# Kernel tuning notes

Measured on AMD Instinct MI355X. Metric: run time of the kernel, lower is better.

## Reference

```python
import jax, jax.numpy as jnp
import numpy as np

H = 16        # num_attention_heads
E = 1024      # hidden_size
D = E // H    # attention_head_size = 64
M = 1024      # max_position_embeddings
EPS = 1e-12


def setup_inputs() -> dict:
    key = jax.random.key(0)
    ks = jax.random.split(key, 12)
    s = 0.02
    B, S = 8, 1024
    return {
        "hidden_states": jax.random.normal(ks[0], (B, S, E), jnp.float32),
        "Wq": jax.random.normal(ks[1], (E, E), jnp.float32) * s,
        "bq": jnp.zeros((E,), jnp.float32),
        "Wk": jax.random.normal(ks[2], (E, E), jnp.float32) * s,
        "bk": jnp.zeros((E,), jnp.float32),
        "Wv": jax.random.normal(ks[3], (E, E), jnp.float32) * s,
        "bv": jnp.zeros((E,), jnp.float32),
        "dist_emb": jax.random.normal(ks[4], (2 * M - 1, D), jnp.float32) * s,
        "Wo": jax.random.normal(ks[5], (E, E), jnp.float32) * s,
        "bo": jnp.zeros((E,), jnp.float32),
        "ln_gamma": jnp.ones((E,), jnp.float32),
        "ln_beta": jnp.zeros((E,), jnp.float32),
    }


def reference(hidden_states, Wq, bq, Wk, bk, Wv, bv, dist_emb, Wo, bo, ln_gamma, ln_beta):
    B, S, _ = hidden_states.shape

    def heads(x):  # [B,S,E] -> [B,H,S,D]
        return x.reshape(B, S, H, D).transpose(0, 2, 1, 3)

    q = heads(hidden_states @ Wq + bq)
    k = heads(hidden_states @ Wk + bk)
    v = heads(hidden_states @ Wv + bv)

    scores = jnp.einsum("bhqd,bhkd->bhqk", q, k)

    # relative_key_query positional bias
    pos_l = jnp.arange(S)[:, None]
    pos_r = jnp.arange(S)[None, :]
    dist_idx = pos_l - pos_r + M - 1            # [S,S] in [0, 2M-2]
    pos_emb = dist_emb[dist_idx]                # [S,S,D]  (l, r, d)
    rel_q = jnp.einsum("bhld,lrd->bhlr", q, pos_emb)
    rel_k = jnp.einsum("bhrd,lrd->bhlr", k, pos_emb)
    scores = (scores + rel_q + rel_k) / jnp.sqrt(jnp.asarray(D, scores.dtype))

    probs = jax.nn.softmax(scores, axis=-1)     # dropout prob = 0 (eval)
    ctx = jnp.einsum("bhqk,bhkd->bhqd", probs, v)
    ctx = ctx.transpose(0, 2, 1, 3).reshape(B, S, E)

    # BertSelfOutput: dense + residual + LayerNorm
    h = ctx @ Wo + bo + hidden_states
    mu = jnp.mean(h, axis=-1, keepdims=True)
    var = jnp.mean(jnp.square(h - mu), axis=-1, keepdims=True)
    out = (h - mu) * jax.lax.rsqrt(var + EPS) * ln_gamma + ln_beta
    return out
```

## Files before the change

kernel.cpp:

```cpp
#include <hip/hip_runtime.h>


typedef unsigned short u16;
typedef unsigned int u32;
typedef unsigned long long u64;
typedef __bf16 bf16x8 __attribute__((ext_vector_type(8)));
typedef float  f32x4  __attribute__((ext_vector_type(4)));
typedef int    i32x4  __attribute__((ext_vector_type(4)));

__device__ __forceinline__ float b2f(u16 u) {
  union { u32 i; float f; } x;
  x.i = ((u32)u) << 16;
  return x.f;
}
__device__ __forceinline__ u16 f2b_manual(float f) {
  union { float f; u32 u; } x;
  x.f = f;
  return (u16)((x.u + 0x7FFFu + ((x.u >> 16) & 1u)) >> 16);
}
#if __has_builtin(__builtin_amdgcn_cvt_pk_bf16_f32)
typedef __bf16 bf16x2 __attribute__((ext_vector_type(2)));
__device__ __forceinline__ u32 cvt2(float a, float b) {
  union { bf16x2 v; u32 u; } x;
  x.v = __builtin_amdgcn_cvt_pk_bf16_f32(a, b);
  return x.u;
}
#else
__device__ __forceinline__ u32 cvt2(float a, float b) {
  return (u32)f2b_manual(a) | ((u32)f2b_manual(b) << 16);
}
#endif
__device__ __forceinline__ u16 f2b(float f) { return (u16)(cvt2(f, f) & 0xffffu); }

union LdU { i32x4 i4; bf16x8 b8; };
__device__ __forceinline__ bf16x8 ldb8(const u16* p) {
  LdU u; u.i4 = *(const i32x4*)p; return u.b8;
}
__device__ __forceinline__ void pack8(u16* dst, const float* src) {
  f32x4 lo = *(const f32x4*)src, hi = *(const f32x4*)(src + 4);
  i32x4 v;
  v.x = (int)cvt2(lo.x, lo.y); v.y = (int)cvt2(lo.z, lo.w);
  v.z = (int)cvt2(hi.x, hi.y); v.w = (int)cvt2(hi.z, hi.w);
  *(i32x4*)dst = v;
}
#define MFMA16(a, b, c) __builtin_amdgcn_mfma_f32_16x16x32_bf16((a), (b), (c), 0, 0, 0)

template <int C>
__device__ __forceinline__ float dppmov(float x) {
  union { float f; int i; } a, r;
  a.f = x;
  r.i = __builtin_amdgcn_update_dpp(0, a.i, C, 0xF, 0xF, true);
  return r.f;
}
__device__ __forceinline__ float rsum16(float x) {
  x += dppmov<0xB1>(x);
  x += dppmov<0x4E>(x);
  x += dppmov<0x141>(x);
  x += dppmov<0x140>(x);
  return x;
}
__device__ __forceinline__ float fexp2(float x) {
#if __has_builtin(__builtin_amdgcn_exp2f)
  return __builtin_amdgcn_exp2f(x);
#else
  return exp2f(x);
#endif
}

#if __has_builtin(__builtin_amdgcn_global_load_lds)
#define HAS_GLDS 1
typedef __attribute__((address_space(3))) u32 as3_u32;
typedef const __attribute__((address_space(1))) u32 as1_u32;
__device__ __forceinline__ void gld16(const u16* g, u16* lds_wave_base) {
  __builtin_amdgcn_global_load_lds(
      (as1_u32*)g, (as3_u32*)(u32)(u64)lds_wave_base, 16, 0, 0);
}
#else
#define HAS_GLDS 0
__device__ __forceinline__ void gld16_fb(const u16* g, u16* lds_wave_base,
                                         int lane) {
  *(i32x4*)(lds_wave_base + lane * 8) = *(const i32x4*)g;
}
#endif

#define SQRT_C2 0.42466090f

__global__ __launch_bounds__(256) void convX(
    const float* __restrict__ X, u16* __restrict__ Xb) {
  int i = (blockIdx.x * 256 + threadIdx.x) * 8;
  pack8(&Xb[i], &X[i]);
}

__global__ __launch_bounds__(256) void convD(
    const float* __restrict__ dist, u16* __restrict__ distb) {
  int i = (blockIdx.x * 256 + threadIdx.x) * 8;
  if (i < 2047 * 64) {
    float t[8];
#pragma unroll
    for (int j = 0; j < 8; j++) t[j] = dist[i + j] * SQRT_C2;
    pack8(&distb[i], t);
  }
}

__global__ __launch_bounds__(256) void convWt4(
    const float* __restrict__ W0, const float* __restrict__ W1,
    const float* __restrict__ W2, const float* __restrict__ W3,
    u16* __restrict__ Wt) {
  __shared__ float tile[64][65];
  const int tid = threadIdx.x;
  const int k0 = blockIdx.x * 64, m0 = blockIdx.y * 64;
  const int z = blockIdx.z;
  const float* W = (z == 0) ? W0 : (z == 1) ? W1 : (z == 2) ? W2 : W3;
  u16* Wtz = Wt + (size_t)z * 1024 * 1024;
#pragma unroll
  for (int it = 0; it < 4; it++) {
    int row = (tid >> 4) + 16 * it;
    int col = (tid & 15) * 4;
    f32x4 v = *(const f32x4*)&W[(size_t)(k0 + row) * 1024 + m0 + col];
    tile[row][col] = v.x; tile[row][col + 1] = v.y;
    tile[row][col + 2] = v.z; tile[row][col + 3] = v.w;
  }
  __syncthreads();
#pragma unroll
  for (int it = 0; it < 4; it++) {
    int mr = (tid >> 4) + 16 * it;
    int kc = (tid & 15) * 4;
    u32 w0 = cvt2(tile[kc][mr], tile[kc + 1][mr]);
    u32 w1 = cvt2(tile[kc + 2][mr], tile[kc + 3][mr]);
    *(u64*)&Wtz[(size_t)(m0 + mr) * 1024 + k0 + kc] = (u64)w0 | ((u64)w1 << 32);
  }
}

__global__ __launch_bounds__(256) void transV(
    const u16* __restrict__ V, u16* __restrict__ Vt) {
  __shared__ u16 tile[64][72];
  const int tid = threadIdx.x;
  const int bh = blockIdx.y, b = bh >> 4, h = bh & 15;
  const int s0 = blockIdx.x << 6;
  const u16* Vb = V + (size_t)(b * 1024) * 1024 + h * 64;
  {
    int rp = tid >> 3, a = tid & 7;
    const u16* src = &Vb[(size_t)(s0 + 2 * rp) * 1024 + a * 8];
    i32x4 va = *(const i32x4*)src;
    i32x4 vb2 = *(const i32x4*)(src + 1024);
    u16 ta[8] __attribute__((aligned(16)));
    u16 tb[8] __attribute__((aligned(16)));
    *(i32x4*)ta = va; *(i32x4*)tb = vb2;
    int colb = ((((rp >> 2) ^ a) << 3) | ((2 * rp) & 7));
#pragma unroll
    for (int j = 0; j < 8; j++)
      *(u32*)&tile[a * 8 + j][colb] = (u32)ta[j] | ((u32)tb[j] << 16);
  }
  __syncthreads();
  int d = tid >> 2, cc = tid & 3;
  int sw = (d >> 3) & 7;
  i32x4 lo = *(const i32x4*)&tile[d][((2 * cc) ^ sw) << 3];
  i32x4 hi = *(const i32x4*)&tile[d][((2 * cc + 1) ^ sw) << 3];
  u16* dst = Vt + ((size_t)bh * 64 + d) * 1024 + s0 + cc * 16;
  *(i32x4*)dst = lo;
  *(i32x4*)(dst + 8) = hi;
}

template <int RESID, int OUTF32, int QKV>
__global__ __launch_bounds__(256) void gemm_bb(
    const u16* __restrict__ A, const u16* __restrict__ Wt,
    const float* __restrict__ bias, const float* __restrict__ biasK,
    const float* __restrict__ biasV, const float* __restrict__ resid,
    float* __restrict__ outF, u16* __restrict__ outB, int N, int K, int M) {
  __shared__ u16 sA[128 * 64];
  __shared__ u16 sW[128 * 64];

  const int tid = threadIdx.x;
  const int lane = tid & 63, w = tid >> 6;
  const int quad = lane >> 4, lb = lane & 15;
  const int m0 = blockIdx.y * 128, n0 = blockIdx.x * 128;

  const int srow = lane >> 3;
  const int gcol = ((lane & 7) ^ srow) << 3;

  f32x4 acc[2][8] = {};

  for (int k0 = 0; k0 < K; k0 += 64) {
#pragma unroll
    for (int j = 0; j < 4; j++) {
      int rb = (4 * w + j) * 8;
      const u16* ga = &A[(size_t)(n0 + rb + srow) * K + k0 + gcol];
      const u16* gw = &Wt[(size_t)(m0 + rb + srow) * K + k0 + gcol];
#if HAS_GLDS
      gld16(ga, &sA[rb * 64]);
      gld16(gw, &sW[rb * 64]);
#else
      gld16_fb(ga, &sA[rb * 64], lane);
      gld16_fb(gw, &sW[rb * 64], lane);
#endif
    }
    __syncthreads();

    const int r0 = 32 * w + lb;
    const int sw0 = r0 & 7;
    bf16x8 a00 = ldb8(&sA[r0 * 64 + ((quad ^ sw0) << 3)]);
    bf16x8 a01 = ldb8(&sA[r0 * 64 + (((4 + quad) ^ sw0) << 3)]);
    bf16x8 a10 = ldb8(&sA[(r0 + 16) * 64 + ((quad ^ sw0) << 3)]);
    bf16x8 a11 = ldb8(&sA[(r0 + 16) * 64 + (((4 + quad) ^ sw0) << 3)]);
#pragma unroll
    for (int t = 0; t < 8; t++) {
      int n = 16 * t + lb;
      int swn = n & 7;
      bf16x8 b0 = ldb8(&sW[n * 64 + ((quad ^ swn) << 3)]);
      bf16x8 b1 = ldb8(&sW[n * 64 + (((4 + quad) ^ swn) << 3)]);
      acc[0][t] = MFMA16(a00, b0, acc[0][t]);
      acc[0][t] = MFMA16(a01, b1, acc[0][t]);
      acc[1][t] = MFMA16(a10, b0, acc[1][t]);
      acc[1][t] = MFMA16(a11, b1, acc[1][t]);
    }
    __syncthreads();
  }

  const float* bp = bias;
  u16* outSeg = outB;
  float osc = 1.0f;
  int mbase = m0;
  if (QKV) {
    int seg = m0 >> 10;
    bp = (seg == 0) ? bias : (seg == 1) ? biasK : biasV;
    outSeg = outB + (size_t)seg * ((size_t)8192 * 1024);
    osc = (seg < 2) ? SQRT_C2 : 1.0f;
    mbase = m0 & 1023;
  }

#pragma unroll
  for (int half = 0; half < 2; half++)
#pragma unroll
    for (int t = 0; t < 8; t++) {
      int colw = mbase + 16 * t + lb;
      float bv = bp[colw];
#pragma unroll
      for (int i = 0; i < 4; i++) {
        int rowg = n0 + 32 * w + 16 * half + quad * 4 + i;
        float v = acc[half][t][i] + bv;
        if (RESID) v += resid[(size_t)rowg * M + colw];
        if (QKV) v *= osc;
        if (OUTF32) outF[(size_t)rowg * M + colw] = v;
        else        outSeg[(size_t)rowg * (QKV ? 1024 : M) + colw] = f2b(v);
      }
    }
}

__global__ __launch_bounds__(256) void attn(
    const u16* __restrict__ Q, const u16* __restrict__ Kv,
    const u16* __restrict__ Vt, const u16* __restrict__ distb,
    u16* __restrict__ ctx) {
  __shared__ u16 sQ[64][72];
  __shared__ u16 sK[64][72];
  __shared__ u16 sVt[64][72];
  __shared__ u16 sP[128][72];
  __shared__ u16 sGq[128 * 64];
  __shared__ u16 sGk[128 * 64];

  const int tid = threadIdx.x;
  const int lane = tid & 63, w = tid >> 6;
  const int quad = lane >> 4, lb = lane & 15;
  const int f = blockIdx.y * 16 + blockIdx.x;
  const int xcd = f & 7, slot = f >> 3;
  const int bh = (xcd << 4) | (slot & 15);
  const int q0 = (slot >> 4) << 6;
  const int b = bh >> 4, h = bh & 15;
  const int S = 1024, E = 1024;
  const u16* Qb = Q  + (size_t)(b * S) * E + h * 64;
  const u16* Kb = Kv + (size_t)(b * S) * E + h * 64;
  const u16* Vtb = Vt + (size_t)bh * 64 * 1024;

  const int sr = tid >> 3, sc8 = (tid & 7) << 3;

  {
    *(i32x4*)&sQ[sr][sc8] = *(const i32x4*)&Qb[(size_t)(q0 + sr) * E + sc8];
    *(i32x4*)&sQ[sr + 32][sc8] =
        *(const i32x4*)&Qb[(size_t)(q0 + sr + 32) * E + sc8];
    *(i32x4*)&sK[sr][sc8] = *(const i32x4*)&Kb[(size_t)sr * E + sc8];
    *(i32x4*)&sK[sr + 32][sc8] =
        *(const i32x4*)&Kb[(size_t)(sr + 32) * E + sc8];
    *(i32x4*)&sVt[sr][sc8] = *(const i32x4*)&Vtb[(size_t)sr * 1024 + sc8];
    *(i32x4*)&sVt[sr + 32][sc8] =
        *(const i32x4*)&Vtb[(size_t)(sr + 32) * 1024 + sc8];
    const int dbase = q0 + 960;
#pragma unroll
    for (int j = 0; j < 4; j++) {
      int p = sr + 32 * j;
      int g = dbase + p;
      if (g > 2046) g = 2046;
      *(i32x4*)&sP[p][sc8] = *(const i32x4*)&distb[(size_t)g * 64 + sc8];
    }
  }
  __syncthreads();

  const int row = 16 * w + lb;
  bf16x8 aq0 = ldb8(&sQ[row][quad * 8]);
  bf16x8 aq1 = ldb8(&sQ[row][32 + quad * 8]);

  const u16* kb  = &sK[lb][quad * 8];
  const u16* vbp = &sVt[lb][quad * 8];
  const u16* akb = &sK[row][quad * 8];
  const u16* pb  = &sP[lb][quad * 8];
  u16* gqsb = &sGq[lb * 64 + ((16 * w + 4 * quad) ^ ((lb & 7) << 3))];
  u16* gksb = &sGk[lb * 64 + ((16 * w + 4 * quad) ^ ((lb & 7) << 3))];
  u16* psb  = &sK[16 * w + 4 * quad][lb];
  const int rl_ = 16 * w + 4 * quad;
  const u16* gqa_[4];
  const u16* gka_[4][4];
#pragma unroll
  for (int i = 0; i < 4; i++) {
    int rl = rl_ + i;
    int c3 = rl - lb + 15;
    int sw8 = (c3 & 7) << 3;
    gqa_[i] = &sGq[(c3 << 6) + (rl ^ sw8)];
#pragma unroll
    for (int t = 0; t < 4; t++) {
      int c = rl - (16 * t + lb) + 63;
      gka_[i][t] = &sGk[(c << 6) + ((16 * t + lb) ^ sw8)];
    }
  }
  const u16* kg0 = Kb + (size_t)(64 + sr) * E + sc8;
  const u16* kg1 = kg0 + (size_t)32 * E;
  const u16* vg0 = Vtb + (size_t)sr * 1024 + 64 + sc8;
  const u16* vg1 = vg0 + (size_t)32 * 1024;
  const u16* dg0 = distb + (size_t)(q0 - 64 + 960 + sr) * 64 + sc8;
  const u16* dg1 = dg0 + (size_t)32 * 64;
  u16* wk0 = &sK[sr][sc8];  u16* wk1 = &sK[sr + 32][sc8];
  u16* wv0 = &sVt[sr][sc8]; u16* wv1 = &sVt[sr + 32][sc8];
  u16* wp0 = &sP[sr][sc8];  u16* wp1 = &sP[sr + 32][sc8];

  const int uqlo = w, uqhi = w + 4;
  const int uklo = 3 - w, ukhi = 7 - w;

  f32x4 accO[4] = {};
  float l_i[4] = {0.f, 0.f, 0.f, 0.f};

  for (int kt = 0; kt < 16; kt++) {
    const int xorv = (kt & 1) << 6;

    i32x4 kr0, kr1, vr0, vr1, dr0, dr1;
    if (kt < 15) {
      kr0 = *(const i32x4*)kg0;
      kr1 = *(const i32x4*)kg1;
      vr0 = *(const i32x4*)vg0;
      vr1 = *(const i32x4*)vg1;
      dr0 = *(const i32x4*)dg0;
      dr1 = *(const i32x4*)dg1;
    }

    __builtin_amdgcn_s_setprio(1);
    f32x4 accS[4] = {};
#pragma unroll
    for (int t = 0; t < 4; t++) {
      bf16x8 b0 = ldb8(kb + 1152 * t);
      bf16x8 b1 = ldb8(kb + 1152 * t + 32);
      accS[t] = MFMA16(aq0, b0, accS[t]);
      accS[t] = MFMA16(aq1, b1, accS[t]);
    }
    bf16x8 ak0 = ldb8(akb);
    bf16x8 ak1 = ldb8(akb + 32);
    const u16* pbA = pb + (xorv ? 4608 : 0);
    const u16* pbB = pb + (xorv ? -4608 : 0);
#pragma unroll
    for (int u = 0; u < 8; u++) {
      const bool doq = (u >= uqlo) && (u <= uqhi);
      const bool dok = (u >= uklo) && (u <= ukhi);
      if (doq || dok) {
        const u16* pp = (u < 4 ? pbA : pbB) + 1152 * u;
        bf16x8 p0 = ldb8(pp);
        bf16x8 p1 = ldb8(pp + 32);
        if (doq) {
          f32x4 gq = {};
          gq = MFMA16(aq0, p0, gq);
          gq = MFMA16(aq1, p1, gq);
          *(u32*)(gqsb + 1024 * u) = cvt2(gq[0], gq[1]);
          *(u32*)(gqsb + 1024 * u + 2) = cvt2(gq[2], gq[3]);
        }
        if (dok) {
          f32x4 gk = {};
          gk = MFMA16(ak0, p0, gk);
          gk = MFMA16(ak1, p1, gk);
          *(u32*)(gksb + 1024 * u) = cvt2(gk[0], gk[1]);
          *(u32*)(gksb + 1024 * u + 2) = cvt2(gk[2], gk[3]);
        }
      }
    }
    __builtin_amdgcn_s_setprio(0);
    __syncthreads();

    float pr[4][4];
#pragma unroll
    for (int t = 0; t < 4; t++) {
#pragma unroll
      for (int i = 0; i < 4; i++) {
        float s = accS[t][i] + b2f(gqa_[i][1024 * (3 - t)]) +
                  b2f(*gka_[i][t]);
        float e = fexp2(s);
        pr[t][i] = e;
        l_i[i] += e;
      }
    }

#pragma unroll
    for (int t = 0; t < 4; t++)
#pragma unroll
      for (int i = 0; i < 4; i++)
        psb[72 * i + 16 * t] = f2b(pr[t][i]);

    bf16x8 ap0 = ldb8(akb);
    bf16x8 ap1 = ldb8(akb + 32);
    __builtin_amdgcn_s_setprio(1);
#pragma unroll
    for (int t = 0; t < 4; t++) {
      bf16x8 v0 = ldb8(vbp + 1152 * t);
      bf16x8 v1 = ldb8(vbp + 1152 * t + 32);
      accO[t] = MFMA16(ap0, v0, accO[t]);
      accO[t] = MFMA16(ap1, v1, accO[t]);
    }
    __builtin_amdgcn_s_setprio(0);
    __syncthreads();

    if (kt < 15) {
      const int pxn = ((kt + 1) & 1) ? 4608 : 0;
      *(i32x4*)wk0 = kr0;
      *(i32x4*)wk1 = kr1;
      *(i32x4*)wv0 = vr0;
      *(i32x4*)wv1 = vr1;
      *(i32x4*)(wp0 + pxn) = dr0;
      *(i32x4*)(wp1 + pxn) = dr1;
      kg0 += (size_t)64 * E; kg1 += (size_t)64 * E;
      vg0 += 64;             vg1 += 64;
      dg0 -= 64 * 64;        dg1 -= 64 * 64;
      __syncthreads();
    }
  }

#pragma unroll
  for (int i = 0; i < 4; i++) l_i[i] = rsum16(l_i[i]);

  u16* Cb = ctx + (size_t)(b * S) * E + h * 64;
#pragma unroll
  for (int t = 0; t < 4; t++)
#pragma unroll
    for (int i = 0; i < 4; i++) {
      int rl = 16 * w + quad * 4 + i;
      Cb[(size_t)(q0 + rl) * E + 16 * t + lb] = f2b(accO[t][i] / l_i[i]);
    }
}

__global__ __launch_bounds__(256) void lnorm(
    const float* __restrict__ Hp, const float* __restrict__ gamma,
    const float* __restrict__ beta, float* __restrict__ out) {
  __shared__ float red[8];
  const int rowb = blockIdx.x, tid = threadIdx.x;
  const float* hr = Hp + (size_t)rowb * 1024;
  f32x4 v = *(const f32x4*)&hr[tid * 4];
  float s = v.x + v.y + v.z + v.w;
  float q = v.x * v.x + v.y * v.y + v.z * v.z + v.w * v.w;
#pragma unroll
  for (int d = 1; d < 64; d <<= 1) {
    s += __shfl_xor(s, d, 64);
    q += __shfl_xor(q, d, 64);
  }
  int w = tid >> 6, lane = tid & 63;
  if (lane == 0) { red[w] = s; red[4 + w] = q; }
  __syncthreads();
  s = red[0] + red[1] + red[2] + red[3];
  q = red[4] + red[5] + red[6] + red[7];
  float mu = s * (1.f / 1024.f);
  float var = q * (1.f / 1024.f) - mu * mu;
  float rstd = rsqrtf(var + 1e-12f);
  float* orow = out + (size_t)rowb * 1024;
  f32x4 o;
#pragma unroll
  for (int j = 0; j < 4; j++) {
    int c = tid * 4 + j;
    o[j] = (v[j] - mu) * rstd * gamma[c] + beta[c];
  }
  *(f32x4*)&orow[tid * 4] = o;
}

extern "C" void kernel_launch(void* const* d_in, const int* in_sizes, int n_in,
                              void* d_out, int out_size, void* d_ws,
                              size_t ws_size, hipStream_t stream) {
  const float* X    = (const float*)d_in[0];
  const float* Wq   = (const float*)d_in[1];
  const float* bq   = (const float*)d_in[2];
  const float* Wk   = (const float*)d_in[3];
  const float* bk   = (const float*)d_in[4];
  const float* Wv   = (const float*)d_in[5];
  const float* bv   = (const float*)d_in[6];
  const float* dist = (const float*)d_in[7];
  const float* Wo   = (const float*)d_in[8];
  const float* bo   = (const float*)d_in[9];
  const float* gam  = (const float*)d_in[10];
  const float* bet  = (const float*)d_in[11];

  const size_t NE = (size_t)8192 * 1024;
  char* ws = (char*)d_ws;
  u16* Qw = (u16*)(ws);
  u16* Kw = (u16*)(ws + 2 * NE);
  u16* Vw = (u16*)(ws + 4 * NE);
  u16* Cw = (u16*)(ws + 6 * NE);
  float* Hp = (float*)ws;

  char* ob = (char*)d_out;
  u16* Wt4 = (u16*)(ob);
  u16* Wto = (u16*)(ob + (6u << 20));
  u16* Xb  = (u16*)(ob + (8u << 20));
  u16* Vtg = (u16*)(ob + (8u << 20));
  u16* distb = (u16*)(ob + (26u << 20));

  dim3 bb(256);
  convWt4<<<dim3(16, 16, 4), bb, 0, stream>>>(Wq, Wk, Wv, Wo, Wt4);
  convX<<<dim3(4096), bb, 0, stream>>>(X, Xb);
  convD<<<dim3(64), bb, 0, stream>>>(dist, distb);

  gemm_bb<0, 0, 1><<<dim3(64, 24), bb, 0, stream>>>(
      Xb, Wt4, bq, bk, bv, nullptr, nullptr, Qw, 8192, 1024, 3072);
  transV<<<dim3(16, 128), bb, 0, stream>>>(Vw, Vtg);
  attn<<<dim3(16, 128), bb, 0, stream>>>(Qw, Kw, Vtg, distb, Cw);
  gemm_bb<1, 1, 0><<<dim3(64, 8), bb, 0, stream>>>(
      Cw, Wto, bo, nullptr, nullptr, X, Hp, nullptr, 8192, 1024, 1024);
  lnorm<<<dim3(8192), bb, 0, stream>>>(Hp, gam, bet, (float*)d_out);
}
```

Baseline: 406.5 us.

## Shrink attention LDS footprint via XOR-swizzled layouts and aliased Q buffer

Replaces the padded [64][72] layouts of V^T and the distance-embedding tile with unpadded 64-wide rows that use an XOR swizzle to avoid bank conflicts. The Gq/Gk scratch shrinks from 128 to 80 rows by offsetting per-wave indices, and the Q staging buffer is aliased onto sGk because Q is only read once into registers. The smaller shared-memory footprint is meant to let more blocks reside per CU. The risk is indexing errors in the rebased Gq/Gk offsets and the aliasing.

```diff
diff --git a/kernel.cpp b/kernel.cpp
--- a/kernel.cpp
+++ b/kernel.cpp
@@ -250,12 +250,11 @@
     const u16* __restrict__ Q, const u16* __restrict__ Kv,
     const u16* __restrict__ Vt, const u16* __restrict__ distb,
     u16* __restrict__ ctx) {
-  __shared__ u16 sQ[64][72];
   __shared__ u16 sK[64][72];
-  __shared__ u16 sVt[64][72];
-  __shared__ u16 sP[128][72];
-  __shared__ u16 sGq[128 * 64];
-  __shared__ u16 sGk[128 * 64];
+  __shared__ u16 sVt[64 * 64];
+  __shared__ u16 sP[128 * 64];
+  __shared__ u16 sGq[80 * 64];
+  __shared__ u16 sGk[80 * 64];
 
   const int tid = threadIdx.x;
   const int lane = tid & 63, w = tid >> 6;
@@ -270,17 +269,19 @@
   const u16* Kb = Kv + (size_t)(b * S) * E + h * 64;
   const u16* Vtb = Vt + (size_t)bh * 64 * 1024;
 
-  const int sr = tid >> 3, sc8 = (tid & 7) << 3;
+  const int sr = tid >> 3, g8 = tid & 7, sc8 = g8 << 3;
+  const int vswz = (g8 ^ (sr & 7)) << 3;
 
   {
+    u16(*sQ)[72] = (u16(*)[72])sGk;
     *(i32x4*)&sQ[sr][sc8] = *(const i32x4*)&Qb[(size_t)(q0 + sr) * E + sc8];
     *(i32x4*)&sQ[sr + 32][sc8] =
         *(const i32x4*)&Qb[(size_t)(q0 + sr + 32) * E + sc8];
     *(i32x4*)&sK[sr][sc8] = *(const i32x4*)&Kb[(size_t)sr * E + sc8];
     *(i32x4*)&sK[sr + 32][sc8] =
         *(const i32x4*)&Kb[(size_t)(sr + 32) * E + sc8];
-    *(i32x4*)&sVt[sr][sc8] = *(const i32x4*)&Vtb[(size_t)sr * 1024 + sc8];
-    *(i32x4*)&sVt[sr + 32][sc8] =
+    *(i32x4*)&sVt[sr * 64 + vswz] = *(const i32x4*)&Vtb[(size_t)sr * 1024 + sc8];
+    *(i32x4*)&sVt[(sr + 32) * 64 + vswz] =
         *(const i32x4*)&Vtb[(size_t)(sr + 32) * 1024 + sc8];
     const int dbase = q0 + 960;
 #pragma unroll
@@ -288,21 +289,29 @@
       int p = sr + 32 * j;
       int g = dbase + p;
       if (g > 2046) g = 2046;
-      *(i32x4*)&sP[p][sc8] = *(const i32x4*)&distb[(size_t)g * 64 + sc8];
+      *(i32x4*)&sP[p * 64 + vswz] = *(const i32x4*)&distb[(size_t)g * 64 + sc8];
     }
   }
   __syncthreads();
 
   const int row = 16 * w + lb;
-  bf16x8 aq0 = ldb8(&sQ[row][quad * 8]);
-  bf16x8 aq1 = ldb8(&sQ[row][32 + quad * 8]);
-
-  const u16* kb  = &sK[lb][quad * 8];
-  const u16* vbp = &sVt[lb][quad * 8];
+  bf16x8 aq0, aq1;
+  {
+    u16(*sQ)[72] = (u16(*)[72])sGk;
+    aq0 = ldb8(&sQ[row][quad * 8]);
+    aq1 = ldb8(&sQ[row][32 + quad * 8]);
+  }
+
+  const int lsw = (lb & 7) << 3;
+  const u16* kb   = &sK[lb][quad * 8];
+  const u16* vbp0 = &sVt[lb * 64 + ((quad ^ (lb & 7)) << 3)];
+  const u16* vbp1 = &sVt[lb * 64 + (((4 + quad) ^ (lb & 7)) << 3)];
   const u16* akb = &sK[row][quad * 8];
-  const u16* pb  = &sP[lb][quad * 8];
-  u16* gqsb = &sGq[lb * 64 + ((16 * w + 4 * quad) ^ ((lb & 7) << 3))];
-  u16* gksb = &sGk[lb * 64 + ((16 * w + 4 * quad) ^ ((lb & 7) << 3))];
+  const u16* pb0 = &sP[lb * 64 + ((quad ^ (lb & 7)) << 3)];
+  const u16* pb1 = &sP[lb * 64 + (((4 + quad) ^ (lb & 7)) << 3)];
+  const int cswz = (16 * w + 4 * quad) ^ lsw;
+  u16* gqsb = sGq + (lb * 64 + cswz - 1024 * w);
+  u16* gksb = sGk + (lb * 64 + cswz + 1024 * w - 3072);
   u16* psb  = &sK[16 * w + 4 * quad][lb];
   const int rl_ = 16 * w + 4 * quad;
   const u16* gqa_[4];
@@ -312,12 +321,11 @@
     int rl = rl_ + i;
     int c3 = rl - lb + 15;
     int sw8 = (c3 & 7) << 3;
-    gqa_[i] = &sGq[(c3 << 6) + (rl ^ sw8)];
-#pragma unroll
-    for (int t = 0; t < 4; t++) {
-      int c = rl - (16 * t + lb) + 63;
-      gka_[i][t] = &sGk[(c << 6) + ((16 * t + lb) ^ sw8)];
-    }
+    gqa_[i] = &sGq[((c3 - 16 * w) << 6) + (rl ^ sw8)];
+    int pk = rl - lb + 15;
+#pragma unroll
+    for (int t = 0; t < 4; t++)
+      gka_[i][t] = &sGk[(pk << 6) + ((16 * t + lb) ^ sw8)];
   }
   const u16* kg0 = Kb + (size_t)(64 + sr) * E + sc8;
   const u16* kg1 = kg0 + (size_t)32 * E;
@@ -325,9 +333,9 @@
   const u16* vg1 = vg0 + (size_t)32 * 1024;
   const u16* dg0 = distb + (size_t)(q0 - 64 + 960 + sr) * 64 + sc8;
   const u16* dg1 = dg0 + (size_t)32 * 64;
-  u16* wk0 = &sK[sr][sc8];  u16* wk1 = &sK[sr + 32][sc8];
-  u16* wv0 = &sVt[sr][sc8]; u16* wv1 = &sVt[sr + 32][sc8];
-  u16* wp0 = &sP[sr][sc8];  u16* wp1 = &sP[sr + 32][sc8];
+  u16* wk0 = &sK[sr][sc8];        u16* wk1 = &sK[sr + 32][sc8];
+  u16* wv0 = &sVt[sr * 64 + vswz]; u16* wv1 = wv0 + 2048;
+  u16* wp0 = &sP[sr * 64 + vswz];  u16* wp1 = wp0 + 2048;
 
   const int uqlo = w, uqhi = w + 4;
   const int uklo = 3 - w, ukhi = 7 - w;
@@ -359,16 +367,17 @@
     }
     bf16x8 ak0 = ldb8(akb);
     bf16x8 ak1 = ldb8(akb + 32);
-    const u16* pbA = pb + (xorv ? 4608 : 0);
-    const u16* pbB = pb + (xorv ? -4608 : 0);
+    const u16* pA0 = pb0 + (xorv ? 4096 : 0);
+    const u16* pA1 = pb1 + (xorv ? 4096 : 0);
+    const u16* pB0 = pb0 + (xorv ? -4096 : 0);
+    const u16* pB1 = pb1 + (xorv ? -4096 : 0);
 #pragma unroll
     for (int u = 0; u < 8; u++) {
       const bool doq = (u >= uqlo) && (u <= uqhi);
       const bool dok = (u >= uklo) && (u <= ukhi);
       if (doq || dok) {
-        const u16* pp = (u < 4 ? pbA : pbB) + 1152 * u;
-        bf16x8 p0 = ldb8(pp);
-        bf16x8 p1 = ldb8(pp + 32);
+        bf16x8 p0 = ldb8((u < 4 ? pA0 : pB0) + 1024 * u);
+        bf16x8 p1 = ldb8((u < 4 ? pA1 : pB1) + 1024 * u);
         if (doq) {
           f32x4 gq = {};
           gq = MFMA16(aq0, p0, gq);
@@ -412,8 +421,8 @@
     __builtin_amdgcn_s_setprio(1);
 #pragma unroll
     for (int t = 0; t < 4; t++) {
-      bf16x8 v0 = ldb8(vbp + 1152 * t);
-      bf16x8 v1 = ldb8(vbp + 1152 * t + 32);
+      bf16x8 v0 = ldb8(vbp0 + 1024 * t);
+      bf16x8 v1 = ldb8(vbp1 + 1024 * t);
       accO[t] = MFMA16(ap0, v0, accO[t]);
       accO[t] = MFMA16(ap1, v1, accO[t]);
     }
@@ -421,7 +430,7 @@
     __syncthreads();
 
     if (kt < 15) {
-      const int pxn = ((kt + 1) & 1) ? 4608 : 0;
+      const int pxn = ((kt + 1) & 1) ? 4096 : 0;
       *(i32x4*)wk0 = kr0;
       *(i32x4*)wk1 = kr1;
       *(i32x4*)wv0 = vr0;
```

After: 409.0 us. No clear change (+0.6%).
